# Kernel optimization log

Measured on AMD Instinct MI355X. Metric: run time of the kernel, lower is better.

## Reference

```python
import jax, jax.numpy as jnp
import numpy as np

B, HR, WR, C = 64, 64, 64, 256
NH, WS, SS = 8, 8, 4
HD = C // NH
N = WS * WS
NW = (HR // WS) * (WR // WS)
CRPB_H = 384
MLP_H = 4 * C
EPS = 1e-5


def _rel_tables():
    r = np.arange(-(WS - 1), WS, dtype=np.float32)
    tbl = np.stack(np.meshgrid(r, r, indexing='ij'), axis=-1)[None]  # (1,2W-1,2W-1,2)
    tbl = tbl / (WS - 1)
    tbl = tbl * 8.0
    tbl = np.sign(tbl) * np.log2(np.abs(tbl) + 1.0) / np.log2(8.0)
    ch, cw = np.meshgrid(np.arange(WS), np.arange(WS), indexing='ij')
    coords = np.stack([ch.ravel(), cw.ravel()])            # (2, N)
    rel = (coords[:, :, None] - coords[:, None, :]).transpose(1, 2, 0)
    rel[:, :, 0] += WS - 1
    rel[:, :, 1] += WS - 1
    rel[:, :, 0] *= 2 * WS - 1
    idx = rel.sum(-1)                                      # (N, N)
    return jnp.asarray(tbl, jnp.float32), jnp.asarray(idx, jnp.int32)


def _attn_mask():
    img = np.zeros((HR, WR), np.float32)
    cnt = 0
    sl = [slice(0, -WS), slice(-WS, -SS), slice(-SS, None)]
    for h in sl:
        for w in sl:
            img[h, w] = cnt
            cnt += 1
    mw = img.reshape(HR // WS, WS, WR // WS, WS).transpose(0, 2, 1, 3).reshape(-1, N)
    diff = mw[:, None, :] - mw[:, :, None]
    return jnp.asarray(np.where(diff != 0, -100.0, 0.0).astype(np.float32))


_REL_TBL, _REL_IDX = _rel_tables()
_MASK = _attn_mask()


def _ln(x, w, b):
    m = jnp.mean(x, axis=-1, keepdims=True)
    v = jnp.mean((x - m) ** 2, axis=-1, keepdims=True)
    return (x - m) / jnp.sqrt(v + EPS) * w + b


def setup_inputs() -> dict:
    key = jax.random.key(0)
    ks = jax.random.split(key, 20)
    s = 0.02
    return {
        'x': jax.random.normal(ks[0], (B, HR * WR, C), jnp.float32),
        'qkv_w': jax.random.normal(ks[1], (3 * C, C), jnp.float32) * s,
        'qkv_b': jnp.zeros((3 * C,), jnp.float32),
        'proj_w': jax.random.normal(ks[2], (C, C), jnp.float32) * s,
        'proj_b': jnp.zeros((C,), jnp.float32),
        't_scale': jnp.log(10.0 * jnp.ones((NH, 1, 1), jnp.float32)),
        'crpb_w1': jax.random.normal(ks[3], (CRPB_H, 2), jnp.float32) * s,
        'crpb_b1': jnp.zeros((CRPB_H,), jnp.float32),
        'crpb_w2': jax.random.normal(ks[4], (NH, CRPB_H), jnp.float32) * s,
        'norm1_w': jnp.ones((C,), jnp.float32),
        'norm1_b': jnp.zeros((C,), jnp.float32),
        'norm2_w': jnp.ones((C,), jnp.float32),
        'norm2_b': jnp.zeros((C,), jnp.float32),
        'fc1_w': jax.random.normal(ks[5], (MLP_H, C), jnp.float32) * s,
        'fc1_b': jnp.zeros((MLP_H,), jnp.float32),
        'fc2_w': jax.random.normal(ks[6], (C, MLP_H), jnp.float32) * s,
        'fc2_b': jnp.zeros((C,), jnp.float32),
    }


def reference(x, qkv_w, qkv_b, proj_w, proj_b, t_scale, crpb_w1, crpb_b1,
              crpb_w2, norm1_w, norm1_b, norm2_w, norm2_b,
              fc1_w, fc1_b, fc2_w, fc2_b):
    shortcut = x
    xi = x.reshape(B, HR, WR, C)
    # cyclic shift
    xi = jnp.roll(xi, shift=(-SS, -SS), axis=(1, 2))
    # window partition -> (B*nW, N, C)
    xw = xi.reshape(B, HR // WS, WS, WR // WS, WS, C)
    xw = xw.transpose(0, 1, 3, 2, 4, 5).reshape(-1, N, C)
    Bw = xw.shape[0]

    # qkv
    qkv = xw @ qkv_w.T + qkv_b                       # (Bw, N, 3C)
    qkv = qkv.reshape(Bw, N, 3, NH, HD).transpose(2, 0, 3, 1, 4)
    q, k, v = qkv[0], qkv[1], qkv[2]                 # (Bw, NH, N, HD)

    # cosine attention with clamped learned temperature
    qn = q / jnp.clip(jnp.linalg.norm(q, axis=-1, keepdims=True), 1e-12)
    kn = k / jnp.clip(jnp.linalg.norm(k, axis=-1, keepdims=True), 1e-12)
    scale = jnp.exp(jnp.minimum(t_scale, jnp.log(1.0 / 0.01)))  # (NH,1,1)
    attn = jnp.einsum('bhnd,bhmd->bhnm', qn, kn) * scale

    # continuous relative position bias via MLP + gather
    h = jax.nn.relu(_REL_TBL @ crpb_w1.T + crpb_b1)            # (1,2W-1,2W-1,384)
    table = (h @ crpb_w2.T).reshape(-1, NH)                    # ((2W-1)^2, NH)
    bias = table[_REL_IDX.reshape(-1)].reshape(N, N, NH).transpose(2, 0, 1)
    bias = 16.0 * jax.nn.sigmoid(bias)
    attn = attn + bias[None]

    # shifted-window mask
    attn = attn.reshape(B, NW, NH, N, N) + _MASK[None, :, None]
    attn = jax.nn.softmax(attn.reshape(Bw, NH, N, N), axis=-1)

    out = jnp.einsum('bhnm,bhmd->bhnd', attn, v)
    out = out.transpose(0, 2, 1, 3).reshape(Bw, N, C)
    out = out @ proj_w.T + proj_b

    # window reverse + reverse shift
    out = out.reshape(B, HR // WS, WR // WS, WS, WS, C)
    out = out.transpose(0, 1, 3, 2, 4, 5).reshape(B, HR, WR, C)
    out = jnp.roll(out, shift=(SS, SS), axis=(1, 2)).reshape(B, HR * WR, C)

    # Swin-V2 post-norm residuals
    xo = shortcut + _ln(out, norm1_w, norm1_b)
    m = jax.nn.gelu(xo @ fc1_w.T + fc1_b, approximate=False)
    m = m @ fc2_w.T + fc2_b
    return xo + _ln(m, norm2_w, norm2_b)
```

## Files before the change

kernel.cpp:

```cpp
#include <hip/hip_runtime.h>

typedef float f32x4 __attribute__((ext_vector_type(4)));
typedef _Float16 f16;
typedef _Float16 f16x8 __attribute__((ext_vector_type(8)));
typedef unsigned int u32;
typedef unsigned short u16;

__device__ __forceinline__ u16 f2h(float f){
  f16 h = (f16)f; return __builtin_bit_cast(u16, h);
}
__device__ __forceinline__ float h2f(u16 u){
  f16 h = __builtin_bit_cast(f16, u); return (float)h;
}
__device__ __forceinline__ f16x8 ld16(const void* p){
  uint4 v = *(const uint4*)p;
  return __builtin_bit_cast(f16x8, v);
}
__device__ __forceinline__ f32x4 mm(f16x8 a, f16x8 b, f32x4 c){
  return __builtin_amdgcn_mfma_f32_16x16x32_f16(a, b, c, 0, 0, 0);
}

__global__ void k_wconv(const float* __restrict__ qkvw, const float* __restrict__ projw,
                        const float* __restrict__ fc1w, const float* __restrict__ fc2w,
                        u16* __restrict__ o_qkv, u16* __restrict__ o_proj,
                        u16* __restrict__ o_fc1, u16* __restrict__ o_fc2){
  int t = blockIdx.x*256 + threadIdx.x;
  int frag = t >> 6, lane = t & 63;
  int l15 = lane & 15, g = lane >> 4;
  const float* src; u16* dst; int col, k, ld, f;
  if(frag < 384){
    f = frag;
    int part = f >> 7, rem = f & 127;
    int h = rem >> 4, rem2 = rem & 15;
    int tc = rem2 >> 3, kk = rem2 & 7;
    col = part*256 + h*32 + tc*16 + l15; k = kk*32 + g*8;
    src = qkvw; dst = o_qkv; ld = 256;
  } else if(frag < 512){
    f = frag - 384;
    int w8 = f >> 4, rem = f & 15;
    int tn2 = rem >> 3, kk = rem & 7;
    col = w8*32 + tn2*16 + l15; k = kk*32 + g*8;
    src = projw; dst = o_proj; ld = 256;
  } else if(frag < 1024){
    f = frag - 512;
    int ck = f >> 6, rem = f & 63;
    int wn = rem >> 4, rem2 = rem & 15;
    int tn = rem2 >> 3, kk = rem2 & 7;
    col = ck*128 + wn*32 + tn*16 + l15; k = kk*32 + g*8;
    src = fc1w; dst = o_fc1; ld = 256;
  } else {
    f = frag - 1024;
    int wn = f >> 7, rem = f & 127;
    int tn = rem >> 5, rem2 = rem & 31;
    int ck = rem2 >> 2, kk2 = rem2 & 3;
    col = wn*64 + tn*16 + l15; k = ck*128 + kk2*32 + g*8;
    src = fc2w; dst = o_fc2; ld = 1024;
  }
  float4 a = *(const float4*)(src + (size_t)col*ld + k);
  float4 b4 = *(const float4*)(src + (size_t)col*ld + k + 4);
  ushort4 h0, h1;
  h0.x=f2h(a.x); h0.y=f2h(a.y); h0.z=f2h(a.z); h0.w=f2h(a.w);
  h1.x=f2h(b4.x); h1.y=f2h(b4.y); h1.z=f2h(b4.z); h1.w=f2h(b4.w);
  u16* o = dst + (size_t)f*512 + lane*8;
  *(ushort4*)o = h0;
  *(ushort4*)(o+4) = h1;
}

__global__ void k_bias(const float* __restrict__ w1, const float* __restrict__ b1,
                       const float* __restrict__ w2, float* __restrict__ bias){
  __shared__ float tab[225][8];
  int t = threadIdx.x;
  if(t < 225){
    int i15 = t/15, j15 = t%15;
    float di = (float)(i15-7) * (8.f/7.f);
    float dj = (float)(j15-7) * (8.f/7.f);
    float vi = copysignf(log2f(fabsf(di)+1.f)*(1.f/3.f), di);
    float vj = copysignf(log2f(fabsf(dj)+1.f)*(1.f/3.f), dj);
    float acc[8];
    #pragma unroll
    for(int h=0;h<8;h++) acc[h]=0.f;
    for(int c=0;c<384;c++){
      float hv = vi*w1[c*2] + vj*w1[c*2+1] + b1[c];
      hv = fmaxf(hv, 0.f);
      #pragma unroll
      for(int h=0;h<8;h++) acc[h] += hv * w2[h*384+c];
    }
    #pragma unroll
    for(int h=0;h<8;h++) tab[t][h] = acc[h];
  }
  __syncthreads();
  for(int pr = t; pr < 4096; pr += 256){
    int i = pr>>6, j = pr&63;
    int dh = (i>>3)-(j>>3)+7, dw = (i&7)-(j&7)+7;
    int idx = dh*15+dw;
    #pragma unroll
    for(int h=0;h<8;h++){
      float v = tab[idx][h];
      bias[(h*64+i)*64+j] = 16.f / (1.f + __expf(-v));
    }
  }
}

__global__ __launch_bounds__(512, 1)
void k_attn(const float* __restrict__ x, const u16* __restrict__ qkvw,
            const float* __restrict__ qkvb, const u16* __restrict__ projw,
            const float* __restrict__ projb, const float* __restrict__ tsc,
            const float* __restrict__ biastab,
            const float* __restrict__ n1w, const float* __restrict__ n1b,
            u16* __restrict__ y)
{
  extern __shared__ char sm[];
  const int tid = threadIdx.x;
  const int w = tid >> 6, lane = tid & 63;
  const int l15 = lane & 15, g = lane >> 4;
  const int blk = blockIdx.x;
  const int b = blk >> 6, nw = blk & 63, wh = nw >> 3, wwi = nw & 7;

  char* Wq = sm + 32768 + w*12288;
  char* Wk = Wq + 4096;
  char* Wv = Wq + 8192;
  char* Wp = Wq;
  float* nrmq = (float*)(sm + 131072 + w*512);
  float* nrmk = nrmq + 64;

  {
    int row = tid >> 3, seg = tid & 7;
    int hs = ((wh<<3) + (row>>3) + 4) & 63;
    int ws_ = ((wwi<<3) + (row&7) + 4) & 63;
    const float* src = x + (size_t)(b*4096 + hs*64 + ws_)*256 + seg*32;
    char* drow = sm + row*512;
    int sw = (row & 7) << 4;
    #pragma unroll
    for(int u=0; u<4; u++){
      float4 f0 = ((const float4*)src)[2*u];
      float4 f1 = ((const float4*)src)[2*u+1];
      uint4 pk;
      pk.x = (u32)f2h(f0.x) | ((u32)f2h(f0.y)<<16);
      pk.y = (u32)f2h(f0.z) | ((u32)f2h(f0.w)<<16);
      pk.z = (u32)f2h(f1.x) | ((u32)f2h(f1.y)<<16);
      pk.w = (u32)f2h(f1.z) | ((u32)f2h(f1.w)<<16);
      *(uint4*)(drow + (((seg<<6) + (u<<4)) ^ sw)) = pk;
    }
  }
  __syncthreads();

  const int h = w;
  #pragma unroll
  for(int part=0; part<3; part++){
    f32x4 acc[2][4] = {};
    #pragma unroll
    for(int kk=0; kk<8; kk++){
      f16x8 a[4];
      #pragma unroll
      for(int tm=0; tm<4; tm++){
        int row = tm*16 + l15;
        a[tm] = ld16(sm + row*512 + (((kk<<6) + (g<<4)) ^ ((row&7)<<4)));
      }
      #pragma unroll
      for(int tc=0; tc<2; tc++){
        f16x8 bf = ld16(qkvw + (size_t)(part*128 + h*16 + tc*8 + kk)*512 + lane*8);
        #pragma unroll
        for(int tm=0; tm<4; tm++) acc[tc][tm] = mm(a[tm], bf, acc[tc][tm]);
      }
    }
    #pragma unroll
    for(int tc=0; tc<2; tc++){
      float bv = qkvb[part*256 + h*32 + tc*16 + l15];
      #pragma unroll
      for(int tm=0; tm<4; tm++){
        #pragma unroll
        for(int r=0; r<4; r++){
          float val = acc[tc][tm][r] + bv;
          int tok = tm*16 + g*4 + r;
          int col = tc*16 + l15;
          u16 hv = f2h(val);
          if(part==0)      *(u16*)(Wq + (tok<<6) + ((col<<1) ^ ((tok&3)<<4))) = hv;
          else if(part==1) *(u16*)(Wk + (tok<<6) + ((col<<1) ^ ((tok&3)<<4))) = hv;
          else             *(u16*)(Wv + (col<<7) + ((tok<<1) ^ ((col&7)<<4))) = hv;
        }
      }
    }
  }

  {
    float sq = 0.f, sk = 0.f;
    #pragma unroll
    for(int cb=0; cb<4; cb++){
      f16x8 qv = ld16(Wq + (lane<<6) + ((cb<<4) ^ ((lane&3)<<4)));
      f16x8 kv = ld16(Wk + (lane<<6) + ((cb<<4) ^ ((lane&3)<<4)));
      #pragma unroll
      for(int j=0;j<8;j++){ float a=(float)qv[j]; sq+=a*a; float c=(float)kv[j]; sk+=c*c; }
    }
    float sc = __expf(fminf(tsc[h], 4.605170185988091f));
    nrmq[lane] = sc / fmaxf(sqrtf(sq), 1e-12f);
    nrmk[lane] = 1.f / fmaxf(sqrtf(sk), 1e-12f);
  }
  __syncthreads();

  f32x4 s[4][4];
  float rsum[4][4];
  {
    f16x8 qf[4], kf[4];
    #pragma unroll
    for(int tm=0; tm<4; tm++){
      int row = tm*16 + l15;
      qf[tm] = ld16(Wq + (row<<6) + ((g<<4) ^ ((row&3)<<4)));
      kf[tm] = ld16(Wk + (row<<6) + ((g<<4) ^ ((row&3)<<4)));
    }
    const f32x4 z4 = {0.f,0.f,0.f,0.f};
    #pragma unroll
    for(int tm=0; tm<4; tm++)
      #pragma unroll
      for(int tn=0; tn<4; tn++)
        s[tm][tn] = mm(qf[tm], kf[tn], z4);
  }
  {
    int idj[4]; float nk[4];
    #pragma unroll
    for(int tn=0; tn<4; tn++){
      int j = tn*16 + l15;
      nk[tn] = nrmk[j];
      int hsj = (wh<<3) + (j>>3), wsj = (wwi<<3) + (j&7);
      idj[tn] = 3*((hsj<56)?0:((hsj<60)?1:2)) + ((wsj<56)?0:((wsj<60)?1:2));
    }
    #pragma unroll
    for(int tm=0; tm<4; tm++){
      #pragma unroll
      for(int r=0; r<4; r++){
        int i = tm*16 + g*4 + r;
        float nq = nrmq[i];
        int hsi = (wh<<3) + (i>>3), wsi = (wwi<<3) + (i&7);
        int idi = 3*((hsi<56)?0:((hsi<60)?1:2)) + ((wsi<56)?0:((wsi<60)?1:2));
        float vr[4];
        #pragma unroll
        for(int tn=0; tn<4; tn++){
          int j = tn*16 + l15;
          float bv = biastab[((h<<6)+i)*64 + j];
          vr[tn] = s[tm][tn][r]*nq*nk[tn] + bv + ((idi!=idj[tn]) ? -100.f : 0.f);
        }
        float mx = fmaxf(fmaxf(vr[0],vr[1]), fmaxf(vr[2],vr[3]));
        mx = fmaxf(mx, __shfl_xor(mx, 1));
        mx = fmaxf(mx, __shfl_xor(mx, 2));
        mx = fmaxf(mx, __shfl_xor(mx, 4));
        mx = fmaxf(mx, __shfl_xor(mx, 8));
        float sumv = 0.f;
        #pragma unroll
        for(int tn=0; tn<4; tn++){
          float p = exp2f((vr[tn]-mx)*1.4426950408889634f);
          sumv += p;
          vr[tn] = p;
        }
        sumv += __shfl_xor(sumv, 1);
        sumv += __shfl_xor(sumv, 2);
        sumv += __shfl_xor(sumv, 4);
        sumv += __shfl_xor(sumv, 8);
        rsum[tm][r] = sumv;
        #pragma unroll
        for(int tn=0; tn<4; tn++){
          int j = tn*16 + l15;
          *(u16*)(Wp + (i<<7) + ((j<<1) ^ ((i&7)<<4))) = f2h(vr[tn]);
        }
      }
    }
  }
  f32x4 o[4][2] = {};
  #pragma unroll
  for(int kk=0; kk<2; kk++){
    f16x8 pf[4];
    #pragma unroll
    for(int tm=0; tm<4; tm++){
      int row = tm*16 + l15;
      pf[tm] = ld16(Wp + (row<<7) + (((kk<<6)+(g<<4)) ^ ((row&7)<<4)));
    }
    #pragma unroll
    for(int tn=0; tn<2; tn++){
      int n = tn*16 + l15;
      f16x8 vf = ld16(Wv + (n<<7) + (((kk<<6)+(g<<4)) ^ ((n&7)<<4)));
      #pragma unroll
      for(int tm=0; tm<4; tm++) o[tm][tn] = mm(pf[tm], vf, o[tm][tn]);
    }
  }
  #pragma unroll
  for(int tm=0; tm<4; tm++)
    #pragma unroll
    for(int tn=0; tn<2; tn++)
      #pragma unroll
      for(int r=0; r<4; r++){
        int i = tm*16 + g*4 + r;
        int col = h*32 + tn*16 + l15;
        float val = o[tm][tn][r] / rsum[tm][r];
        *(u16*)(sm + (i<<9) + ((col<<1) ^ ((i&7)<<4))) = f2h(val);
      }
  __syncthreads();

  {
    float* yr32 = (float*)(sm + 32768);
    f32x4 pa[4][2] = {};
    #pragma unroll
    for(int kk=0; kk<8; kk++){
      f16x8 a[4];
      #pragma unroll
      for(int tm=0; tm<4; tm++){
        int row = tm*16 + l15;
        a[tm] = ld16(sm + (row<<9) + (((kk<<6)+(g<<4)) ^ ((row&7)<<4)));
      }
      #pragma unroll
      for(int tn=0; tn<2; tn++){
        f16x8 bf = ld16(projw + (size_t)(w*16 + tn*8 + kk)*512 + lane*8);
        #pragma unroll
        for(int tm=0; tm<4; tm++) pa[tm][tn] = mm(a[tm], bf, pa[tm][tn]);
      }
    }
    #pragma unroll
    for(int tn=0; tn<2; tn++){
      float pb = projb[w*32 + tn*16 + l15];
      #pragma unroll
      for(int tm=0; tm<4; tm++)
        #pragma unroll
        for(int r=0; r<4; r++){
          int tok = tm*16 + g*4 + r;
          int col = w*32 + tn*16 + l15;
          yr32[tok*256 + (col ^ ((tok&7)<<2))] = pa[tm][tn][r] + pb;
        }
    }
  }
  __syncthreads();

  {
    int row = tid >> 3, seg = tid & 7;
    const float* yr = (const float*)(sm + 32768) + row*256;
    int sw4 = (row&7)<<2;
    float yv[32];
    float s1 = 0.f, s2 = 0.f;
    #pragma unroll
    for(int t=0; t<8; t++){
      float4 v4 = *(const float4*)(yr + ((seg*32 + t*4) ^ sw4));
      yv[t*4+0]=v4.x; yv[t*4+1]=v4.y; yv[t*4+2]=v4.z; yv[t*4+3]=v4.w;
      s1 += v4.x+v4.y+v4.z+v4.w;
      s2 += v4.x*v4.x+v4.y*v4.y+v4.z*v4.z+v4.w*v4.w;
    }
    s1 += __shfl_xor(s1,1); s2 += __shfl_xor(s2,1);
    s1 += __shfl_xor(s1,2); s2 += __shfl_xor(s2,2);
    s1 += __shfl_xor(s1,4); s2 += __shfl_xor(s2,4);
    float mean = s1*(1.f/256.f);
    float var = s2*(1.f/256.f) - mean*mean;
    float rstd = rsqrtf(var + 1e-5f);
    u32 hw[16];
    #pragma unroll
    for(int j=0; j<32; j++){
      int c = seg*32 + j;
      float zz = (yv[j]-mean)*rstd*n1w[c] + n1b[c];
      u16 hv = f2h(zz);
      if(j&1) hw[j>>1] |= ((u32)hv)<<16; else hw[j>>1] = (u32)hv;
    }
    int ho = ((wh<<3) + (row>>3) + 4) & 63;
    int wo = ((wwi<<3) + (row&7) + 4) & 63;
    u16* dst = y + (size_t)(b*4096 + ho*64 + wo)*256 + seg*32;
    #pragma unroll
    for(int u2=0; u2<4; u2++)
      ((uint4*)dst)[u2] = *(uint4*)(&hw[u2*4]);
  }
}

__global__ __attribute__((amdgpu_waves_per_eu(4,4))) __launch_bounds__(512)
void k_mlp(const float* __restrict__ x, const u16* __restrict__ z,
           const u16* __restrict__ fc1, const float* __restrict__ f1b,
           const u16* __restrict__ fc2, const float* __restrict__ f2bb,
           const float* __restrict__ n2w, const float* __restrict__ n2b,
           float* __restrict__ out)
{
  __shared__ char smem[49152];
  char* xo16 = smem;
  char* hbf  = smem + 32768;
  const int tid = threadIdx.x;
  const int wv = tid>>6, lane = tid&63, l15 = lane&15, g = lane>>4;
  const int wm = wv>>2, wn = wv&3;
  const size_t row0 = (size_t)blockIdx.x * 64;

  {
    int row = tid>>3, seg = tid&7;
    size_t grow = row0 + row;
    const u16* zp = z + grow*256 + seg*32;
    const float* xp = x + grow*256 + seg*32;
    int swb = (row&7)<<4;
    #pragma unroll
    for(int u=0;u<4;u++){
      uint4 raw = ((const uint4*)zp)[u];
      float4 xa = ((const float4*)xp)[2*u];
      float4 xb = ((const float4*)xp)[2*u+1];
      u32 rw[4] = {raw.x, raw.y, raw.z, raw.w};
      float v[8];
      v[0] = xa.x + h2f((u16)(rw[0] & 0xFFFFu));
      v[1] = xa.y + h2f((u16)(rw[0] >> 16));
      v[2] = xa.z + h2f((u16)(rw[1] & 0xFFFFu));
      v[3] = xa.w + h2f((u16)(rw[1] >> 16));
      v[4] = xb.x + h2f((u16)(rw[2] & 0xFFFFu));
      v[5] = xb.y + h2f((u16)(rw[2] >> 16));
      v[6] = xb.z + h2f((u16)(rw[3] & 0xFFFFu));
      v[7] = xb.w + h2f((u16)(rw[3] >> 16));
      u32 pw[4];
      #pragma unroll
      for(int j=0;j<8;j++){
        if(j&1) pw[j>>1] |= ((u32)f2h(v[j]))<<16; else pw[j>>1] = (u32)f2h(v[j]);
      }
      uint4 pk; pk.x=pw[0]; pk.y=pw[1]; pk.z=pw[2]; pk.w=pw[3];
      *(uint4*)(xo16 + (row<<9) + (((seg<<6)+(u<<4)) ^ swb)) = pk;
    }
  }
  __syncthreads();

  f32x4 acc2[2][4] = {};
  for(int ck=0; ck<8; ck++){
    f32x4 a1[2][2] = {{{0.f,0.f,0.f,0.f},{0.f,0.f,0.f,0.f}},
                      {{0.f,0.f,0.f,0.f},{0.f,0.f,0.f,0.f}}};
    {
      const u16* fb = fc1 + ((size_t)(ck*64 + wn*16))*512 + (size_t)lane*8;
      f16x8 bc0 = ld16(fb);
      f16x8 bc1 = ld16(fb + 8*512);
      #pragma unroll
      for(int kk=0; kk<8; kk++){
        f16x8 nb0, nb1;
        if(kk < 7){
          nb0 = ld16(fb + (size_t)(kk+1)*512);
          nb1 = ld16(fb + (size_t)(8+kk+1)*512);
        }
        f16x8 af0, af1;
        {
          int row = wm*32 + l15;
          af0 = ld16(xo16 + (row<<9) + (((kk<<6)+(g<<4)) ^ ((row&7)<<4)));
          row = wm*32 + 16 + l15;
          af1 = ld16(xo16 + (row<<9) + (((kk<<6)+(g<<4)) ^ ((row&7)<<4)));
        }
        a1[0][0] = mm(af0, bc0, a1[0][0]);
        a1[1][0] = mm(af1, bc0, a1[1][0]);
        a1[0][1] = mm(af0, bc1, a1[0][1]);
        a1[1][1] = mm(af1, bc1, a1[1][1]);
        bc0 = nb0; bc1 = nb1;
      }
    }
    #pragma unroll
    for(int tn=0;tn<2;tn++){
      float bv = f1b[ck*128 + wn*32 + tn*16 + l15];
      #pragma unroll
      for(int tm=0;tm<2;tm++)
        #pragma unroll
        for(int r=0;r<4;r++){
          float zv = a1[tm][tn][r] + bv;
          float u0 = 0.7978845608028654f*(zv + 0.044715f*zv*zv*zv);
          float e = exp2f(u0 * 2.8853900817779268f);
          float th = 1.f - 2.f/(e+1.f);
          float ge = 0.5f*zv*(1.f+th);
          int row = wm*32 + tm*16 + g*4 + r;
          int hc = wn*32 + tn*16 + l15;
          *(u16*)(hbf + (row<<8) + ((hc<<1) ^ ((row&7)<<4))) = f2h(ge);
        }
    }
    __syncthreads();
    {
      const u16* gb = fc2 + ((size_t)(wn*128 + ck*4))*512 + (size_t)lane*8;
      f16x8 c0 = ld16(gb);
      f16x8 c1 = ld16(gb + 32*512);
      f16x8 c2 = ld16(gb + 64*512);
      f16x8 c3 = ld16(gb + 96*512);
      #pragma unroll
      for(int kk2=0; kk2<4; kk2++){
        f16x8 n0,n1,n2,n3;
        if(kk2 < 3){
          n0 = ld16(gb + (size_t)(kk2+1)*512);
          n1 = ld16(gb + (size_t)(32+kk2+1)*512);
          n2 = ld16(gb + (size_t)(64+kk2+1)*512);
          n3 = ld16(gb + (size_t)(96+kk2+1)*512);
        }
        f16x8 af0, af1;
        {
          int row = wm*32 + l15;
          af0 = ld16(hbf + (row<<8) + (((kk2<<6)+(g<<4)) ^ ((row&7)<<4)));
          row = wm*32 + 16 + l15;
          af1 = ld16(hbf + (row<<8) + (((kk2<<6)+(g<<4)) ^ ((row&7)<<4)));
        }
        acc2[0][0] = mm(af0, c0, acc2[0][0]);
        acc2[1][0] = mm(af1, c0, acc2[1][0]);
        acc2[0][1] = mm(af0, c1, acc2[0][1]);
        acc2[1][1] = mm(af1, c1, acc2[1][1]);
        acc2[0][2] = mm(af0, c2, acc2[0][2]);
        acc2[1][2] = mm(af1, c2, acc2[1][2]);
        acc2[0][3] = mm(af0, c3, acc2[0][3]);
        acc2[1][3] = mm(af1, c3, acc2[1][3]);
        c0=n0; c1=n1; c2=n2; c3=n3;
      }
    }
    __syncthreads();
  }

  {
    float b2v[4], w2v[4], b2n[4];
    #pragma unroll
    for(int tn=0;tn<4;tn++){
      int col = wn*64 + tn*16 + l15;
      b2v[tn] = f2bb[col];
      w2v[tn] = n2w[col];
      b2n[tn] = n2b[col];
    }
    #pragma unroll
    for(int tm=0;tm<2;tm++)
      #pragma unroll
      for(int tn=0;tn<4;tn++)
        #pragma unroll
        for(int r=0;r<4;r++) acc2[tm][tn][r] += b2v[tn];

    float* lnp = (float*)hbf;
    #pragma unroll
    for(int tm=0;tm<2;tm++)
      #pragma unroll
      for(int r=0;r<4;r++){
        float sA=0.f, sB=0.f;
        #pragma unroll
        for(int tn=0;tn<4;tn++){ float v=acc2[tm][tn][r]; sA+=v; sB+=v*v; }
        sA += __shfl_xor(sA,1); sB += __shfl_xor(sB,1);
        sA += __shfl_xor(sA,2); sB += __shfl_xor(sB,2);
        sA += __shfl_xor(sA,4); sB += __shfl_xor(sB,4);
        sA += __shfl_xor(sA,8); sB += __shfl_xor(sB,8);
        if(l15==0){
          int row = wm*32 + tm*16 + g*4 + r;
          lnp[(row*4+wn)*2]   = sA;
          lnp[(row*4+wn)*2+1] = sB;
        }
      }
    __syncthreads();
    #pragma unroll
    for(int tm=0;tm<2;tm++)
      #pragma unroll
      for(int r=0;r<4;r++){
        int row = wm*32 + tm*16 + g*4 + r;
        float S=0.f, SS=0.f;
        #pragma unroll
        for(int q2=0;q2<4;q2++){ S += lnp[(row*4+q2)*2]; SS += lnp[(row*4+q2)*2+1]; }
        float mean = S*(1.f/256.f);
        float var = SS*(1.f/256.f) - mean*mean;
        float rstd = rsqrtf(var + 1e-5f);
        float* op = out + (row0 + row)*256;
        #pragma unroll
        for(int tn=0;tn<4;tn++){
          int col = wn*64 + tn*16 + l15;
          float xo = h2f(*(const u16*)(xo16 + (row<<9) + ((col<<1) ^ ((row&7)<<4))));
          op[col] = xo + (acc2[tm][tn][r]-mean)*rstd*w2v[tn] + b2n[tn];
        }
      }
  }
}

extern "C" void kernel_launch(void* const* d_in, const int* in_sizes, int n_in,
                              void* d_out, int out_size, void* d_ws, size_t ws_size,
                              hipStream_t stream)
{
  const float* x     = (const float*)d_in[0];
  const float* qkvw  = (const float*)d_in[1];
  const float* qkvb  = (const float*)d_in[2];
  const float* projw = (const float*)d_in[3];
  const float* projb = (const float*)d_in[4];
  const float* tsc   = (const float*)d_in[5];
  const float* w1    = (const float*)d_in[6];
  const float* b1    = (const float*)d_in[7];
  const float* w2    = (const float*)d_in[8];
  const float* n1w   = (const float*)d_in[9];
  const float* n1b   = (const float*)d_in[10];
  const float* n2w   = (const float*)d_in[11];
  const float* n2b   = (const float*)d_in[12];
  const float* fc1w  = (const float*)d_in[13];
  const float* fc1b  = (const float*)d_in[14];
  const float* fc2w  = (const float*)d_in[15];
  const float* fc2b  = (const float*)d_in[16];
  float* out = (float*)d_out;

  char* ws = (char*)d_ws;
  const size_t WB = 134217728;
  u16* z_h      = (u16*)(ws);
  u16* qkvw_h   = (u16*)(ws + WB);
  u16* projw_h  = (u16*)(ws + WB + 393216);
  u16* fc1_h    = (u16*)(ws + WB + 524288);
  u16* fc2_h    = (u16*)(ws + WB + 1048576);
  float* biastab= (float*)(ws + WB + 1572864);

  (void)hipFuncSetAttribute((const void*)k_attn,
                      hipFuncAttributeMaxDynamicSharedMemorySize, 135168);

  k_wconv<<<384, 256, 0, stream>>>(qkvw, projw, fc1w, fc2w,
                                   qkvw_h, projw_h, fc1_h, fc2_h);
  k_bias<<<1, 256, 0, stream>>>(w1, b1, w2, biastab);
  k_attn<<<4096, 512, 135168, stream>>>(x, qkvw_h, qkvb, projw_h, projb,
                                        tsc, biastab, n1w, n1b, z_h);
  k_mlp<<<4096, 512, 0, stream>>>(x, z_h, fc1_h, fc1b,
                                  fc2_h, fc2b, n2w, n2b, out);
}
```

Before: 1.041 ms.

## Split MLP kernel work across 16 waves per block with narrower N tiles

Doubles the k_mlp block from 512 to 1024 threads (16 waves), so each wave owns half as many output columns in both the fc1 and fc2 GEMMs. The fc1 weight pre-pack layout changes to match the 16-column-per-wave tiling. The LayerNorm reduction now spans 8 column groups, and the GELU tanh arithmetic is lightly rewritten. The aim is more latency hiding and lower per-wave register pressure, at the cost of fewer MFMAs per A-fragment load (less reuse) and heavier block-level synchronisation.

```diff
diff --git a/kernel.cpp b/kernel.cpp
--- a/kernel.cpp
+++ b/kernel.cpp
@@ -44,9 +44,8 @@
   } else if(frag < 1024){
     f = frag - 512;
     int ck = f >> 6, rem = f & 63;
-    int wn = rem >> 4, rem2 = rem & 15;
-    int tn = rem2 >> 3, kk = rem2 & 7;
-    col = ck*128 + wn*32 + tn*16 + l15; k = kk*32 + g*8;
+    int wn8 = rem >> 3, kk = rem & 7;
+    col = ck*128 + wn8*16 + l15; k = kk*32 + g*8;
     src = fc1w; dst = o_fc1; ld = 256;
   } else {
     f = frag - 1024;
@@ -362,7 +361,7 @@
   }
 }
 
-__global__ __attribute__((amdgpu_waves_per_eu(4,4))) __launch_bounds__(512)
+__global__ __launch_bounds__(1024, 4)
 void k_mlp(const float* __restrict__ x, const u16* __restrict__ z,
            const u16* __restrict__ fc1, const float* __restrict__ f1b,
            const u16* __restrict__ fc2, const float* __restrict__ f2bb,
@@ -374,17 +373,17 @@
   char* hbf  = smem + 32768;
   const int tid = threadIdx.x;
   const int wv = tid>>6, lane = tid&63, l15 = lane&15, g = lane>>4;
-  const int wm = wv>>2, wn = wv&3;
+  const int wm = wv>>3, wn = wv&7;
   const size_t row0 = (size_t)blockIdx.x * 64;
 
   {
-    int row = tid>>3, seg = tid&7;
+    int row = tid>>4, s16 = tid&15;
     size_t grow = row0 + row;
-    const u16* zp = z + grow*256 + seg*32;
-    const float* xp = x + grow*256 + seg*32;
+    const u16* zp = z + grow*256 + s16*16;
+    const float* xp = x + grow*256 + s16*16;
     int swb = (row&7)<<4;
     #pragma unroll
-    for(int u=0;u<4;u++){
+    for(int u=0;u<2;u++){
       uint4 raw = ((const uint4*)zp)[u];
       float4 xa = ((const float4*)xp)[2*u];
       float4 xb = ((const float4*)xp)[2*u+1];
@@ -404,26 +403,21 @@
         if(j&1) pw[j>>1] |= ((u32)f2h(v[j]))<<16; else pw[j>>1] = (u32)f2h(v[j]);
       }
       uint4 pk; pk.x=pw[0]; pk.y=pw[1]; pk.z=pw[2]; pk.w=pw[3];
-      *(uint4*)(xo16 + (row<<9) + (((seg<<6)+(u<<4)) ^ swb)) = pk;
+      *(uint4*)(xo16 + (row<<9) + (((s16<<5)+(u<<4)) ^ swb)) = pk;
     }
   }
   __syncthreads();
 
-  f32x4 acc2[2][4] = {};
+  f32x4 acc2[2][2] = {};
   for(int ck=0; ck<8; ck++){
-    f32x4 a1[2][2] = {{{0.f,0.f,0.f,0.f},{0.f,0.f,0.f,0.f}},
-                      {{0.f,0.f,0.f,0.f},{0.f,0.f,0.f,0.f}}};
+    f32x4 a1[2] = {{0.f,0.f,0.f,0.f},{0.f,0.f,0.f,0.f}};
     {
-      const u16* fb = fc1 + ((size_t)(ck*64 + wn*16))*512 + (size_t)lane*8;
+      const u16* fb = fc1 + ((size_t)(ck*64 + wn*8))*512 + (size_t)lane*8;
       f16x8 bc0 = ld16(fb);
-      f16x8 bc1 = ld16(fb + 8*512);
       #pragma unroll
       for(int kk=0; kk<8; kk++){
-        f16x8 nb0, nb1;
-        if(kk < 7){
-          nb0 = ld16(fb + (size_t)(kk+1)*512);
-          nb1 = ld16(fb + (size_t)(8+kk+1)*512);
-        }
+        f16x8 nb0;
+        if(kk < 7) nb0 = ld16(fb + (size_t)(kk+1)*512);
         f16x8 af0, af1;
         {
           int row = wm*32 + l15;
@@ -431,45 +425,41 @@
           row = wm*32 + 16 + l15;
           af1 = ld16(xo16 + (row<<9) + (((kk<<6)+(g<<4)) ^ ((row&7)<<4)));
         }
-        a1[0][0] = mm(af0, bc0, a1[0][0]);
-        a1[1][0] = mm(af1, bc0, a1[1][0]);
-        a1[0][1] = mm(af0, bc1, a1[0][1]);
-        a1[1][1] = mm(af1, bc1, a1[1][1]);
-        bc0 = nb0; bc1 = nb1;
-      }
-    }
-    #pragma unroll
-    for(int tn=0;tn<2;tn++){
-      float bv = f1b[ck*128 + wn*32 + tn*16 + l15];
+        a1[0] = mm(af0, bc0, a1[0]);
+        a1[1] = mm(af1, bc0, a1[1]);
+        bc0 = nb0;
+      }
+    }
+    {
+      float bv = f1b[ck*128 + wn*16 + l15];
       #pragma unroll
       for(int tm=0;tm<2;tm++)
         #pragma unroll
         for(int r=0;r<4;r++){
-          float zv = a1[tm][tn][r] + bv;
-          float u0 = 0.7978845608028654f*(zv + 0.044715f*zv*zv*zv);
+          float zv = a1[tm][r] + bv;
+          float z2 = zv*zv;
+          float u0 = zv*(0.7978845608028654f + 0.035677408136300125f*z2);
           float e = exp2f(u0 * 2.8853900817779268f);
-          float th = 1.f - 2.f/(e+1.f);
-          float ge = 0.5f*zv*(1.f+th);
+          float ge = zv - zv*__frcp_rn(e+1.f)*1.0f;
+          ge = zv - 2.f*zv*(0.5f/(e+1.f));
           int row = wm*32 + tm*16 + g*4 + r;
-          int hc = wn*32 + tn*16 + l15;
+          int hc = wn*16 + l15;
           *(u16*)(hbf + (row<<8) + ((hc<<1) ^ ((row&7)<<4))) = f2h(ge);
         }
     }
     __syncthreads();
     {
-      const u16* gb = fc2 + ((size_t)(wn*128 + ck*4))*512 + (size_t)lane*8;
-      f16x8 c0 = ld16(gb);
-      f16x8 c1 = ld16(gb + 32*512);
-      f16x8 c2 = ld16(gb + 64*512);
-      f16x8 c3 = ld16(gb + 96*512);
+      int wnh = wn>>1, wnl = wn&1;
+      const u16* gb0 = fc2 + ((size_t)(wnh*128 + (wnl*2+0)*32 + ck*4))*512 + (size_t)lane*8;
+      const u16* gb1 = fc2 + ((size_t)(wnh*128 + (wnl*2+1)*32 + ck*4))*512 + (size_t)lane*8;
+      f16x8 c0 = ld16(gb0);
+      f16x8 c1 = ld16(gb1);
       #pragma unroll
       for(int kk2=0; kk2<4; kk2++){
-        f16x8 n0,n1,n2,n3;
+        f16x8 n0, n1;
         if(kk2 < 3){
-          n0 = ld16(gb + (size_t)(kk2+1)*512);
-          n1 = ld16(gb + (size_t)(32+kk2+1)*512);
-          n2 = ld16(gb + (size_t)(64+kk2+1)*512);
-          n3 = ld16(gb + (size_t)(96+kk2+1)*512);
+          n0 = ld16(gb0 + (size_t)(kk2+1)*512);
+          n1 = ld16(gb1 + (size_t)(kk2+1)*512);
         }
         f16x8 af0, af1;
         {
@@ -482,21 +472,17 @@
         acc2[1][0] = mm(af1, c0, acc2[1][0]);
         acc2[0][1] = mm(af0, c1, acc2[0][1]);
         acc2[1][1] = mm(af1, c1, acc2[1][1]);
-        acc2[0][2] = mm(af0, c2, acc2[0][2]);
-        acc2[1][2] = mm(af1, c2, acc2[1][2]);
-        acc2[0][3] = mm(af0, c3, acc2[0][3]);
-        acc2[1][3] = mm(af1, c3, acc2[1][3]);
-        c0=n0; c1=n1; c2=n2; c3=n3;
+        c0=n0; c1=n1;
       }
     }
     __syncthreads();
   }
 
   {
-    float b2v[4], w2v[4], b2n[4];
-    #pragma unroll
-    for(int tn=0;tn<4;tn++){
-      int col = wn*64 + tn*16 + l15;
+    float b2v[2], w2v[2], b2n[2];
+    #pragma unroll
+    for(int tn=0;tn<2;tn++){
+      int col = wn*32 + tn*16 + l15;
       b2v[tn] = f2bb[col];
       w2v[tn] = n2w[col];
       b2n[tn] = n2b[col];
@@ -504,7 +490,7 @@
     #pragma unroll
     for(int tm=0;tm<2;tm++)
       #pragma unroll
-      for(int tn=0;tn<4;tn++)
+      for(int tn=0;tn<2;tn++)
         #pragma unroll
         for(int r=0;r<4;r++) acc2[tm][tn][r] += b2v[tn];
 
@@ -513,17 +499,16 @@
     for(int tm=0;tm<2;tm++)
       #pragma unroll
       for(int r=0;r<4;r++){
-        float sA=0.f, sB=0.f;
-        #pragma unroll
-        for(int tn=0;tn<4;tn++){ float v=acc2[tm][tn][r]; sA+=v; sB+=v*v; }
+        float sA = acc2[tm][0][r] + acc2[tm][1][r];
+        float sB = acc2[tm][0][r]*acc2[tm][0][r] + acc2[tm][1][r]*acc2[tm][1][r];
         sA += __shfl_xor(sA,1); sB += __shfl_xor(sB,1);
         sA += __shfl_xor(sA,2); sB += __shfl_xor(sB,2);
         sA += __shfl_xor(sA,4); sB += __shfl_xor(sB,4);
         sA += __shfl_xor(sA,8); sB += __shfl_xor(sB,8);
         if(l15==0){
           int row = wm*32 + tm*16 + g*4 + r;
-          lnp[(row*4+wn)*2]   = sA;
-          lnp[(row*4+wn)*2+1] = sB;
+          lnp[(row*8+wn)*2]   = sA;
+          lnp[(row*8+wn)*2+1] = sB;
         }
       }
     __syncthreads();
@@ -534,14 +519,14 @@
         int row = wm*32 + tm*16 + g*4 + r;
         float S=0.f, SS=0.f;
         #pragma unroll
-        for(int q2=0;q2<4;q2++){ S += lnp[(row*4+q2)*2]; SS += lnp[(row*4+q2)*2+1]; }
+        for(int q2=0;q2<8;q2++){ S += lnp[(row*8+q2)*2]; SS += lnp[(row*8+q2)*2+1]; }
         float mean = S*(1.f/256.f);
         float var = SS*(1.f/256.f) - mean*mean;
         float rstd = rsqrtf(var + 1e-5f);
         float* op = out + (row0 + row)*256;
         #pragma unroll
-        for(int tn=0;tn<4;tn++){
-          int col = wn*64 + tn*16 + l15;
+        for(int tn=0;tn<2;tn++){
+          int col = wn*32 + tn*16 + l15;
           float xo = h2f(*(const u16*)(xo16 + (row<<9) + ((col<<1) ^ ((row&7)<<4))));
           op[col] = xo + (acc2[tm][tn][r]-mean)*rstd*w2v[tn] + b2n[tn];
         }
@@ -589,6 +574,6 @@
   k_bias<<<1, 256, 0, stream>>>(w1, b1, w2, biastab);
   k_attn<<<4096, 512, 135168, stream>>>(x, qkvw_h, qkvb, projw_h, projb,
                                         tsc, biastab, n1w, n1b, z_h);
-  k_mlp<<<4096, 512, 0, stream>>>(x, z_h, fc1_h, fc1b,
-                                  fc2_h, fc2b, n2w, n2b, out);
-}
+  k_mlp<<<4096, 1024, 0, stream>>>(x, z_h, fc1_h, fc1b,
+                                   fc2_h, fc2b, n2w, n2b, out);
+}
```

New measurement: 1.204 ms. 15.7% more time.
